# Optimization experiments

Hardware: AMD Instinct MI355X
Metric: run time of the kernel (lower is better)

## Reference

```python
import jax, jax.numpy as jnp
import numpy as np

# shift search range (matches init_kwargs)
MIN_SX, MAX_SX = -4, 4
MIN_SY, MAX_SY = -4, 4
B, C, H, W = 4, 3, 512, 512


def _shift(x, sx, sy):
    """torch.roll on dims (1,2) of a [C,H,W] tensor, zeroing wrapped rows/cols.

    Equivalent to AutomatedShiftFix.shift: positive sx zeros rows [:sx],
    negative sx zeros rows [sx:]; same for sy on the W axis.
    """
    h, w = x.shape[1], x.shape[2]
    shifted = jnp.roll(x, (sx, sy), axis=(1, 2))
    i = jnp.arange(h)[:, None]   # [H,1]
    j = jnp.arange(w)[None, :]   # [1,W]
    mask_h = jnp.where(sx >= 0, i >= sx, i < h + sx)
    mask_w = jnp.where(sy >= 0, j >= sy, j < w + sy)
    mask = (mask_h & mask_w).astype(x.dtype)  # [H,W]
    return shifted * mask[None]


def _all_shifts():
    sx = jnp.arange(MIN_SX, MAX_SX + 1)
    sy = jnp.arange(MIN_SY, MAX_SY + 1)
    # outer loop over shift_x, inner over shift_y -> 'ij' matches torch ordering
    return jnp.stack(jnp.meshgrid(sx, sy, indexing="ij"), axis=-1).reshape(-1, 2)  # [Ns,2]


def setup_inputs() -> dict:
    key = jax.random.key(0)
    k1, k2 = jax.random.split(key)
    x_ref = jax.random.normal(k1, (B, C, H, W), dtype=jnp.float32)
    x = jax.random.normal(k2, (B, C, H, W), dtype=jnp.float32)
    return {"x_ref": x_ref, "x": x}


def reference(x_ref, x):
    shifts = _all_shifts()  # [Ns,2] int32

    def sims_one(xr, xi):  # xr, xi: [C,H,W]
        # similarity for every candidate shift: sum over (C,H,W) of shifted*ref
        return jax.vmap(lambda s: jnp.sum(_shift(xi, s[0], s[1]) * xr))(shifts)  # [Ns]

    sims = jax.vmap(sims_one)(x_ref, x)          # [B, Ns]
    best = jnp.argmax(sims, axis=1)              # [B]
    best_shifts = shifts[best]                   # [B, 2]
    out = jax.vmap(lambda xi, s: _shift(xi, s[0], s[1]))(x, best_shifts)  # [B,C,H,W]
    return out, best_shifts
```

## Files before the change

kernel.cpp:

```cpp
#include <hip/hip_runtime.h>

#define BB 4
#define CC 3
#define HH 512
#define WW 512
#define NS 81
#define IMG (HH * WW)
#define CHW (CC * IMG)
#define STRIP 32
#define NSTRIP (HH / STRIP)
#define NBLK (BB * CC * NSTRIP * 9)

__device__ double g_part[NBLK][9];
__device__ int    g_best[BB];

#define C4(v, i) ((i) == 0 ? (v).x : (i) == 1 ? (v).y : (i) == 2 ? (v).z : (v).w)

__global__ __launch_bounds__(256, 4) void k_sims(const float* __restrict__ xref,
                                                 const float* __restrict__ x) {
    int bid  = blockIdx.x;
    int sxi  = bid % 9;
    int tmp  = bid / 9;
    int strip = tmp % NSTRIP;
    int bc   = tmp / NSTRIP;
    const float* xp = x    + (size_t)bc * IMG;
    const float* rp = xref + (size_t)bc * IMG;
    int tid  = threadIdx.x;
    int lane = tid & 63;
    int wave = tid >> 6;
    int j0   = lane << 3;
    int sx   = sxi - 4;
    int ip0  = strip * STRIP + wave * 8;

    float acc[9];
#pragma unroll
    for (int s = 0; s < 9; ++s) acc[s] = 0.f;

#pragma unroll
    for (int rr = 0; rr < 8; ++rr) {
        int ip = ip0 + rr;
        int ii = ip + sx;
        if ((unsigned)ii >= HH) continue;

        const float* xrow = xp + ip * WW + j0;
        const float* rrow = rp + ii * WW + j0;
        float4 xa = *(const float4*)(xrow);
        float4 xb = *(const float4*)(xrow + 4);

        const float4* pp = (const float4*)(rrow + (lane == 0  ? 0 : -4));
        const float4* np = (const float4*)(rrow + (lane == 63 ? 0 :  8));
        float4 pv = *pp;
        float4 ra = *(const float4*)(rrow);
        float4 rb = *(const float4*)(rrow + 4);
        float4 nv = *np;
        if (lane == 0)  pv = make_float4(0.f, 0.f, 0.f, 0.f);
        if (lane == 63) nv = make_float4(0.f, 0.f, 0.f, 0.f);

#pragma unroll
        for (int syi = 0; syi < 9; ++syi) {
#pragma unroll
            for (int k = 0; k < 8; ++k) {
                int i = k + syi;
                float wv = (i < 4)  ? C4(pv, i)
                         : (i < 8)  ? C4(ra, i - 4)
                         : (i < 12) ? C4(rb, i - 8)
                         :            C4(nv, i - 12);
                float xv = (k < 4) ? C4(xa, k) : C4(xb, k - 4);
                acc[syi] += xv * wv;
            }
        }
    }

    __shared__ float part[4][9];
#pragma unroll
    for (int s = 0; s < 9; ++s) {
        float v = acc[s];
        for (int off = 32; off; off >>= 1) v += __shfl_down(v, off, 64);
        if (lane == 0) part[wave][s] = v;
    }
    __syncthreads();
    if (tid < 9) {
        g_part[bid][tid] = (double)part[0][tid] + (double)part[1][tid]
                         + (double)part[2][tid] + (double)part[3][tid];
    }
}

__global__ __launch_bounds__(128) void k_reduce(float* __restrict__ outTail) {
    int b = blockIdx.x;
    int t = threadIdx.x;
    __shared__ double vals[NS];
    if (t < NS) {
        int sxi = t / 9;
        int syi = t % 9;
        double s = 0.0;
#pragma unroll
        for (int c = 0; c < CC; ++c)
#pragma unroll
            for (int st = 0; st < NSTRIP; ++st) {
                int bid = ((b * CC + c) * NSTRIP + st) * 9 + sxi;
                s += g_part[bid][syi];
            }
        vals[t] = s;
    }
    __syncthreads();
    if (t == 0) {
        int best = 0;
        double bv = vals[0];
        for (int i = 1; i < NS; ++i)
            if (vals[i] > bv) { bv = vals[i]; best = i; }
        g_best[b] = best;
        outTail[b * 2]     = (float)(best / 9 - 4);
        outTail[b * 2 + 1] = (float)(best % 9 - 4);
    }
}

__global__ __launch_bounds__(256) void k_apply(const float* __restrict__ x,
                                               float* __restrict__ out) {
    int blk = blockIdx.x;
    int bc  = blk >> 8;
    int tid = threadIdx.x;
    int b   = bc / CC;

    int bi = g_best[b];
    int sx = bi / 9 - 4;
    int sy = bi % 9 - 4;

    int row = ((blk & 255) << 1) + (tid >> 7);
    int j0  = (tid & 127) << 2;
    int is  = row - sx;
    float4 v = make_float4(0.f, 0.f, 0.f, 0.f);
    if ((unsigned)is < HH) {
        const float* src = x + (size_t)bc * IMG + is * WW;
        int js0 = j0 - sy;
        if (js0 >= 0 && js0 + 3 < WW) {
            v = *(const float4*)(src + js0);
        } else {
            float* vv = (float*)&v;
#pragma unroll
            for (int k = 0; k < 4; ++k) {
                int js = js0 + k;
                if ((unsigned)js < WW) vv[k] = src[js];
            }
        }
    }
    *(float4*)(out + (size_t)bc * IMG + row * WW + j0) = v;
}

extern "C" void kernel_launch(void* const* d_in, const int* in_sizes, int n_in,
                              void* d_out, int out_size, void* d_ws, size_t ws_size,
                              hipStream_t stream) {
    const float* xref = (const float*)d_in[0];
    const float* x    = (const float*)d_in[1];
    float* out = (float*)d_out;
    (void)d_ws; (void)ws_size;

    k_sims<<<NBLK, 256, 0, stream>>>(xref, x);
    k_reduce<<<BB, 128, 0, stream>>>(out + (size_t)BB * CHW);

    int applyBlocks = (BB * CC * HH) / 2;
    k_apply<<<applyBlocks, 256, 0, stream>>>(x, out);
}
```

Measured before the change: 111.5 us.

## Map all nine vertical shifts to waves of one block and use lane shuffles for halo

Each block now covers a 16-row strip with nine waves, one per vertical shift, so the x rows are shared across waves through cache within a block instead of being spread over separate blocks. Neighbour halo values come from cross-lane shuffles rather than extra global loads. Partial sums are written per wave straight into a slot-major buffer, which removes the shared-memory reduction and barrier and lets the reduce kernel read contiguously. The cost is more rows of serial work per thread and the register pressure of 576-thread blocks.

```diff
diff --git a/kernel.cpp b/kernel.cpp
--- a/kernel.cpp
+++ b/kernel.cpp
@@ -7,37 +7,37 @@
 #define NS 81
 #define IMG (HH * WW)
 #define CHW (CC * IMG)
-#define STRIP 32
-#define NSTRIP (HH / STRIP)
-#define NBLK (BB * CC * NSTRIP * 9)
+#define STRIP 16
+#define NSTRIPS (HH / STRIP)
+#define NBLK (BB * CC * NSTRIPS)
+#define SLOTS (CC * NSTRIPS)
 
-__device__ double g_part[NBLK][9];
+__device__ double g_part[(size_t)BB * NS * SLOTS];
 __device__ int    g_best[BB];
 
 #define C4(v, i) ((i) == 0 ? (v).x : (i) == 1 ? (v).y : (i) == 2 ? (v).z : (v).w)
 
-__global__ __launch_bounds__(256, 4) void k_sims(const float* __restrict__ xref,
-                                                 const float* __restrict__ x) {
-    int bid  = blockIdx.x;
-    int sxi  = bid % 9;
-    int tmp  = bid / 9;
-    int strip = tmp % NSTRIP;
-    int bc   = tmp / NSTRIP;
+__global__ __launch_bounds__(576) void k_sims(const float* __restrict__ xref,
+                                              const float* __restrict__ x) {
+    int bid   = blockIdx.x;
+    int strip = bid % NSTRIPS;
+    int bc    = bid / NSTRIPS;
+    int b     = bc / CC;
     const float* xp = x    + (size_t)bc * IMG;
     const float* rp = xref + (size_t)bc * IMG;
     int tid  = threadIdx.x;
     int lane = tid & 63;
-    int wave = tid >> 6;
+    int sxi  = tid >> 6;
     int j0   = lane << 3;
     int sx   = sxi - 4;
-    int ip0  = strip * STRIP + wave * 8;
+    int ip0  = strip * STRIP;
 
     float acc[9];
 #pragma unroll
     for (int s = 0; s < 9; ++s) acc[s] = 0.f;
 
 #pragma unroll
-    for (int rr = 0; rr < 8; ++rr) {
+    for (int rr = 0; rr < STRIP; ++rr) {
         int ip = ip0 + rr;
         int ii = ip + sx;
         if ((unsigned)ii >= HH) continue;
@@ -46,42 +46,46 @@
         const float* rrow = rp + ii * WW + j0;
         float4 xa = *(const float4*)(xrow);
         float4 xb = *(const float4*)(xrow + 4);
-
-        const float4* pp = (const float4*)(rrow + (lane == 0  ? 0 : -4));
-        const float4* np = (const float4*)(rrow + (lane == 63 ? 0 :  8));
-        float4 pv = *pp;
         float4 ra = *(const float4*)(rrow);
         float4 rb = *(const float4*)(rrow + 4);
-        float4 nv = *np;
-        if (lane == 0)  pv = make_float4(0.f, 0.f, 0.f, 0.f);
-        if (lane == 63) nv = make_float4(0.f, 0.f, 0.f, 0.f);
 
+        float p0 = __shfl_up(rb.x, 1, 64);
+        float p1 = __shfl_up(rb.y, 1, 64);
+        float p2 = __shfl_up(rb.z, 1, 64);
+        float p3 = __shfl_up(rb.w, 1, 64);
+        if (lane == 0) { p0 = p1 = p2 = p3 = 0.f; }
+        float n0 = __shfl_down(ra.x, 1, 64);
+        float n1 = __shfl_down(ra.y, 1, 64);
+        float n2 = __shfl_down(ra.z, 1, 64);
+        float n3 = __shfl_down(ra.w, 1, 64);
+        if (lane == 63) { n0 = n1 = n2 = n3 = 0.f; }
+
+#define P4(i) ((i) == 0 ? p0 : (i) == 1 ? p1 : (i) == 2 ? p2 : p3)
+#define N4(i) ((i) == 0 ? n0 : (i) == 1 ? n1 : (i) == 2 ? n2 : n3)
 #pragma unroll
         for (int syi = 0; syi < 9; ++syi) {
 #pragma unroll
             for (int k = 0; k < 8; ++k) {
                 int i = k + syi;
-                float wv = (i < 4)  ? C4(pv, i)
+                float wv = (i < 4)  ? P4(i)
                          : (i < 8)  ? C4(ra, i - 4)
                          : (i < 12) ? C4(rb, i - 8)
-                         :            C4(nv, i - 12);
+                         :            N4(i - 12);
                 float xv = (k < 4) ? C4(xa, k) : C4(xb, k - 4);
                 acc[syi] += xv * wv;
             }
         }
+#undef P4
+#undef N4
     }
 
-    __shared__ float part[4][9];
+    int cs = (bc % CC) * NSTRIPS + strip;
 #pragma unroll
     for (int s = 0; s < 9; ++s) {
         float v = acc[s];
         for (int off = 32; off; off >>= 1) v += __shfl_down(v, off, 64);
-        if (lane == 0) part[wave][s] = v;
-    }
-    __syncthreads();
-    if (tid < 9) {
-        g_part[bid][tid] = (double)part[0][tid] + (double)part[1][tid]
-                         + (double)part[2][tid] + (double)part[3][tid];
+        if (lane == 0)
+            g_part[((size_t)b * NS + sxi * 9 + s) * SLOTS + cs] = (double)v;
     }
 }
 
@@ -90,16 +94,9 @@
     int t = threadIdx.x;
     __shared__ double vals[NS];
     if (t < NS) {
-        int sxi = t / 9;
-        int syi = t % 9;
+        const double* p = g_part + ((size_t)b * NS + t) * SLOTS;
         double s = 0.0;
-#pragma unroll
-        for (int c = 0; c < CC; ++c)
-#pragma unroll
-            for (int st = 0; st < NSTRIP; ++st) {
-                int bid = ((b * CC + c) * NSTRIP + st) * 9 + sxi;
-                s += g_part[bid][syi];
-            }
+        for (int i = 0; i < SLOTS; ++i) s += p[i];
         vals[t] = s;
     }
     __syncthreads();
@@ -154,7 +151,7 @@
     float* out = (float*)d_out;
     (void)d_ws; (void)ws_size;
 
-    k_sims<<<NBLK, 256, 0, stream>>>(xref, x);
+    k_sims<<<NBLK, 576, 0, stream>>>(xref, x);
     k_reduce<<<BB, 128, 0, stream>>>(out + (size_t)BB * CHW);
 
     int applyBlocks = (BB * CC * HH) / 2;
```

Measured after the change: 96.51 us (median of 2 runs). 13.4% less time.
